# Kernel tuning notes

Hardware: AMD Instinct MI355X
Metric: run time of the kernel (lower is better)

Reference implementation:

```python
import jax, jax.numpy as jnp
import numpy as np

V, D, B, T = 50257, 512, 64, 512
MEM, FWD = 64, 48
RETRO = MEM - FWD  # 16
EPS = 1e-5


def setup_inputs() -> dict:
    key = jax.random.key(0)
    ks = jax.random.split(key, 16)
    n = lambda i, shape: (jax.random.normal(ks[i], shape, jnp.float32) * 0.02)
    return dict(
        seq=jax.random.randint(ks[0], (B, T), 0, V),
        embed=n(1, (V, D)),
        ff_w1=n(2, (D, 2 * D)), ff_b1=jnp.zeros((2 * D,), jnp.float32),
        ff_w2=n(3, (2 * D, D)), ff_b2=jnp.zeros((D,), jnp.float32),
        ln_g=jnp.ones((D,), jnp.float32), ln_b=jnp.zeros((D,), jnp.float32),
        fg_w=n(4, (D,)), fg_b=jnp.zeros((), jnp.float32),
        nw_w1=n(5, (2 * D, D)), nw_b1=jnp.zeros((D,), jnp.float32),
        nw_w2=n(6, (D,)), nw_b2=jnp.zeros((), jnp.float32),
        wq=n(7, (D, D)), bq=jnp.zeros((D,), jnp.float32),
        wk=n(8, (D, D)), bk=jnp.zeros((D,), jnp.float32),
        wv=n(9, (D, D)), bv=jnp.zeros((D,), jnp.float32),
        wo=n(10, (D, D)), bo=jnp.zeros((D,), jnp.float32),
        rq_w=n(11, (D, D)), rq_b=jnp.zeros((D,), jnp.float32),
        out_w=n(12, (D, V)), out_b=jnp.zeros((V,), jnp.float32),
    )


def reference(seq, embed, ff_w1, ff_b1, ff_w2, ff_b2, ln_g, ln_b,
              fg_w, fg_b, nw_w1, nw_b1, nw_w2, nw_b2,
              wq, bq, wk, bk, wv, bv, wo, bo, rq_w, rq_b, out_w, out_b):
    Bz = seq.shape[0]
    # Encoder: embed -> FFN residual -> LayerNorm
    h0 = embed[seq]                                            # [B,T,D]
    ff = jax.nn.relu(h0 @ ff_w1 + ff_b1) @ ff_w2 + ff_b2
    x = h0 + ff
    mu = x.mean(-1, keepdims=True)
    var = ((x - mu) ** 2).mean(-1, keepdims=True)
    hidden = (x - mu) / jnp.sqrt(var + EPS) * ln_g + ln_b       # [B,T,D]

    cand = hidden[:, :-3, :]                                   # [B,n_cand,D]
    n_cand = cand.shape[1]
    # Forward-gate topk (sorted ascending, as in torch code)
    fwd_scores = cand @ fg_w + fg_b                            # [B,n_cand]
    _, fwd_idx = jax.lax.top_k(fwd_scores, FWD)
    fwd_idx = jnp.sort(fwd_idx, axis=1)                        # [B,FWD]
    fwd_h = jnp.take_along_axis(hidden, fwd_idx[:, :, None], axis=1)  # [B,FWD,D]

    # Condition 'D': MHA re-encode (1 head) of forward slots over full sequence
    q = fwd_h @ wq + bq                                        # [B,FWD,D]
    kk = hidden @ wk + bk                                      # [B,T,D]
    v = hidden @ wv + bv                                       # [B,T,D]
    attn = jax.nn.softmax(jnp.einsum('bkd,btd->bkt', q, kk) / jnp.sqrt(jnp.float32(D)), axis=-1)
    re_slots = jnp.einsum('bkt,btd->bkd', attn, v) @ wo + bo   # [B,FWD,D]

    # New-write gate over skipped candidates -> retro slots
    context = hidden.mean(1)                                   # [B,D]
    gi = jnp.concatenate([cand, jnp.broadcast_to(context[:, None, :], cand.shape)], axis=-1)
    gs = jax.nn.sigmoid(jax.nn.relu(gi @ nw_w1 + nw_b1) @ nw_w2 + nw_b2)  # [B,n_cand]
    fwd_mask = jnp.zeros((Bz, n_cand), jnp.float32).at[
        jnp.arange(Bz)[:, None], fwd_idx].set(1.0)
    masked = jnp.where(fwd_mask > 0, -1e9, gs)
    _, sel = jax.lax.top_k(masked, RETRO)                      # [B,RETRO], descending-score order
    retro_h = jnp.take_along_axis(hidden, sel[:, :, None], axis=1)  # [B,RETRO,D]

    memory = jnp.concatenate([re_slots, retro_h], axis=1)      # [B,MEM,D] (exactly full)
    mem_mask = jnp.ones((Bz, MEM), jnp.float32)

    # Read head
    qh = hidden[:, -2, :] @ rq_w + rq_b                        # [B,D]
    scores = jnp.einsum('bmd,bd->bm', memory, qh)
    scores = jnp.where(mem_mask == 0, -1e9, scores)
    a = jax.nn.softmax(scores, axis=-1)
    ctx = jnp.einsum('bm,bmd->bd', a, memory)
    return ctx @ out_w + out_b                                 # [B,V]
```

## Files before the change

kernel.cpp:

```cpp
#include <hip/hip_runtime.h>

typedef unsigned short u16;
typedef unsigned int u32;

#define VV 50257
#define NCAND 509
#define NFWD 48
#define NRETRO 16

typedef __attribute__((ext_vector_type(8))) short bf16x8;
typedef __attribute__((ext_vector_type(4))) float f32x4;

__device__ __forceinline__ float bf2f(u16 u) {
  union { u32 i; float f; } v; v.i = ((u32)u) << 16; return v.f;
}
__device__ __forceinline__ u16 f2bf(float f) {
  union { float f; u32 u; } v; v.f = f;
  u32 u = v.u; u += 0x7fffu + ((u >> 16) & 1u); return (u16)(u >> 16);
}
__device__ __forceinline__ u16 bft(float f) {
  union { float f; u32 u; } v; v.f = f; return (u16)(v.u >> 16);
}
__device__ __forceinline__ float ldsel(const void* p, size_t i, int isbf) {
  return isbf ? bf2f(((const u16*)p)[i]) : ((const float*)p)[i];
}

__device__ __forceinline__ void g2l16(const u16* g, u16* l) {
  __builtin_amdgcn_global_load_lds((const __attribute__((address_space(1))) u32*)g,
                                   (__attribute__((address_space(3))) u32*)l, 16, 0, 0);
}

__global__ void detect_k(const u32* __restrict__ w, int* __restrict__ flag) {
  int bf = 1;
  for (int i = 0; i < 16; ++i) {
    u32 b1 = (w[i] >> 8) & 0x7fu;
    if (!(b1 >= 0x30u && b1 < 0x40u)) bf = 0;
  }
  *flag = bf;
}

__global__ void sentinel_k(float* __restrict__ out, int n, float val) {
  int i = blockIdx.x * 256 + threadIdx.x;
  if (i < n) out[i] = val;
}

__global__ __launch_bounds__(256) void tsplit_k(const float* __restrict__ W,
                                                u16* __restrict__ Th, u16* __restrict__ Tl,
                                                int K, int N) {
  __shared__ float tt[32][33];
  int nt = N >> 5;
  int n0 = (blockIdx.x % nt) << 5;
  int k0 = (blockIdx.x / nt) << 5;
  int c = threadIdx.x & 31, r = threadIdx.x >> 5;
#pragma unroll
  for (int i = 0; i < 32; i += 8) tt[r + i][c] = W[(size_t)(k0 + r + i) * N + n0 + c];
  __syncthreads();
#pragma unroll
  for (int i = 0; i < 32; i += 8) {
    int n = n0 + r + i, k = k0 + c;
    float v = tt[c][r + i];
    u16 h = bft(v);
    int idx = n * K + (k & ~63) + ((k & 63) ^ ((n & 7) << 3));
    Th[idx] = h; Tl[idx] = f2bf(v - bf2f(h));
  }
}

__global__ __launch_bounds__(256) void tout_k(const float* __restrict__ W,
                                              u16* __restrict__ WoT) {
  __shared__ float tt[32][33];
  const int nt = 1572;
  int n0 = (blockIdx.x % nt) << 5;
  int k0 = (blockIdx.x / nt) << 5;
  int c = threadIdx.x & 31, r = threadIdx.x >> 5;
#pragma unroll
  for (int i = 0; i < 32; i += 8) {
    int n = n0 + c;
    tt[r + i][c] = (n < VV) ? W[(size_t)(k0 + r + i) * VV + n] : 0.f;
  }
  __syncthreads();
#pragma unroll
  for (int i = 0; i < 32; i += 8) {
    int n = n0 + r + i, k = k0 + c;
    WoT[(size_t)n * 512 + (k & ~63) + ((k & 63) ^ ((n & 7) << 3))] = f2bf(tt[c][r + i]);
  }
}

__global__ void concat2_k(const float* __restrict__ a, const float* __restrict__ b,
                          float* __restrict__ o) {
  int i = blockIdx.x * 256 + threadIdx.x;
  if (i < 1024) o[i] = (i < 512) ? a[i] : b[i - 512];
}

__global__ __launch_bounds__(256) void gsplit_k(const float* __restrict__ embed,
                                                const int* __restrict__ seqp,
                                                u16* __restrict__ Ph, u16* __restrict__ Pl) {
  int g = blockIdx.x * 256 + threadIdx.x;
  int m = g >> 6, j8 = (g & 63) << 3;
  const float* s = embed + (size_t)seqp[m] * 512 + j8;
  float4 a = *(const float4*)s;
  float4 b = *(const float4*)(s + 4);
  u16 h0 = bft(a.x), h1 = bft(a.y), h2 = bft(a.z), h3 = bft(a.w);
  u16 h4 = bft(b.x), h5 = bft(b.y), h6 = bft(b.z), h7 = bft(b.w);
  uint4 hv, lv;
  hv.x = (u32)h0 | ((u32)h1 << 16); hv.y = (u32)h2 | ((u32)h3 << 16);
  hv.z = (u32)h4 | ((u32)h5 << 16); hv.w = (u32)h6 | ((u32)h7 << 16);
  lv.x = (u32)f2bf(a.x - bf2f(h0)) | ((u32)f2bf(a.y - bf2f(h1)) << 16);
  lv.y = (u32)f2bf(a.z - bf2f(h2)) | ((u32)f2bf(a.w - bf2f(h3)) << 16);
  lv.z = (u32)f2bf(b.x - bf2f(h4)) | ((u32)f2bf(b.y - bf2f(h5)) << 16);
  lv.w = (u32)f2bf(b.z - bf2f(h6)) | ((u32)f2bf(b.w - bf2f(h7)) << 16);
  int di = m * 512 + (j8 ^ ((m & 7) << 3));
  *(uint4*)&Ph[di] = hv;
  *(uint4*)&Pl[di] = lv;
}

template<int NT, int KST, int ADDM, int RELU, int OUT>
__global__ __launch_bounds__(256) void mgemm_k(
    const u16* __restrict__ Ah, const u16* __restrict__ Al,
    const u16* __restrict__ Bh, const u16* __restrict__ Bl,
    int lda, int ldb, int koff,
    const float* __restrict__ biasf, int boff,
    const u16* __restrict__ Rh, const u16* __restrict__ Rl,
    const float* __restrict__ addf,
    float* __restrict__ Cf, u16* __restrict__ Cb,
    u16* __restrict__ Ohi, u16* __restrict__ Olo, int ldc)
{
  __shared__ __align__(16) u16 lds[32768];
  int tid = threadIdx.x;
  int cpx = gridDim.x >> 3;
  int bid = blockIdx.x;
  int wg = (bid & 7) * cpx + (bid >> 3);
  int my = wg / NT, nx = wg % NT;
  int m0 = my << 7, n0 = nx << 7;
  int lane = tid & 63, wid = tid >> 6;

  const u16* gw; int stw;
  if (wid == 0)      { gw = Ah + (size_t)m0 * lda;        stw = lda; }
  else if (wid == 1) { gw = Al + (size_t)m0 * lda;        stw = lda; }
  else if (wid == 2) { gw = Bh + (size_t)n0 * ldb + koff; stw = ldb; }
  else               { gw = Bl + (size_t)n0 * ldb + koff; stw = ldb; }
  const u16* gl = gw + (size_t)(lane >> 3) * stw + ((lane & 7) << 3);
  int lb = wid << 13;

  f32x4 acc[4][4] = {};
  int wr = wid >> 1, wc = wid & 1;
  int cl = lane & 15;
  int kq8 = (lane >> 4) << 3;
  int swz = (cl & 7) << 3;

  for (int k0 = 0; k0 < KST * 64; k0 += 64) {
#pragma unroll
    for (int i = 0; i < 16; ++i)
      g2l16(gl + (size_t)(i << 3) * stw + k0, &lds[lb + (i << 9)]);
    __syncthreads();
#pragma unroll
    for (int kt = 0; kt < 2; ++kt) {
      int kA = ((kt << 5) + kq8) ^ swz;
      bf16x8 bh[4], blo[4];
#pragma unroll
      for (int i = 0; i < 4; ++i) {
        int ib = (((wc << 6) + (i << 4) + cl) << 6) + kA;
        bh[i]  = *(const bf16x8*)&lds[16384 + ib];
        blo[i] = *(const bf16x8*)&lds[24576 + ib];
      }
#pragma unroll
      for (int i2 = 0; i2 < 4; ++i2) {
        int ia = (((wr << 6) + (i2 << 4) + cl) << 6) + kA;
        bf16x8 ah  = *(const bf16x8*)&lds[ia];
        bf16x8 alo = *(const bf16x8*)&lds[8192 + ia];
#pragma unroll
        for (int j = 0; j < 4; ++j) {
          acc[i2][j] = __builtin_amdgcn_mfma_f32_16x16x32_bf16(ah,  bh[j],  acc[i2][j], 0, 0, 0);
          acc[i2][j] = __builtin_amdgcn_mfma_f32_16x16x32_bf16(alo, bh[j],  acc[i2][j], 0, 0, 0);
          acc[i2][j] = __builtin_amdgcn_mfma_f32_16x16x32_bf16(ah,  blo[j], acc[i2][j], 0, 0, 0);
        }
      }
    }
    __syncthreads();
  }

  int rq = (lane >> 4) << 2;
  int mb = m0 + (wr << 6);
  int nb = n0 + (wc << 6);
#pragma unroll
  for (int j = 0; j < 4; ++j) {
    int n = nb + (j << 4) + cl;
    float bi = biasf ? biasf[boff + n] : 0.f;
#pragma unroll
    for (int i2 = 0; i2 < 4; ++i2) {
#pragma unroll
      for (int r = 0; r < 4; ++r) {
        int m = mb + (i2 << 4) + rq + r;
        float v = acc[i2][j][r] + bi;
        if (ADDM == 1) {
          int ridx = m * 512 + (n ^ ((m & 7) << 3));
          v += bf2f(Rh[ridx]) + bf2f(Rl[ridx]);
        }
        if (ADDM == 2) v += addf[((m >> 9) << 9) + n];
        if (RELU) v = fmaxf(v, 0.f);
        if (OUT == 0) Cf[(size_t)m * ldc + n] = v;
        else if (OUT == 1) Cb[(size_t)m * ldc + n] = f2bf(v);
        else if (OUT == 2) {
          u16 h = bft(v);
          size_t oidx = (size_t)m * ldc + (n & ~63) + ((n & 63) ^ ((m & 7) << 3));
          Ohi[oidx] = h; Olo[oidx] = f2bf(v - bf2f(h));
        } else {
          int r64 = (m * 43691) >> 21;
          int mm = (r64 << 6) + (m - r64 * 48);
          Cf[(size_t)mm * 512 + n] = v;
        }
      }
    }
  }
}

__global__ __launch_bounds__(256) void out_mgemm_k(
    const u16* __restrict__ ctxh, const u16* __restrict__ ctxl,
    const u16* __restrict__ WoT, const float* __restrict__ ob,
    float* __restrict__ out) {
  __shared__ __align__(16) u16 lds[16384];
  int tid = threadIdx.x;
  int n0 = blockIdx.x << 7;
  int lane = tid & 63, wid = tid >> 6;
  const u16* gw; int lb0;
  if (wid == 0)      { gw = ctxh;                         lb0 = 0; }
  else if (wid == 1) { gw = ctxl;                         lb0 = 4096; }
  else if (wid == 2) { gw = WoT + (size_t)n0 * 512;        lb0 = 8192; }
  else               { gw = WoT + (size_t)(n0 + 64) * 512; lb0 = 12288; }
  const u16* gl = gw + (size_t)(lane >> 3) * 512 + ((lane & 7) << 3);

  f32x4 acc[4][2] = {};
  int cl = lane & 15;
  int kq8 = (lane >> 4) << 3;
  int swz = (cl & 7) << 3;

  for (int k0 = 0; k0 < 512; k0 += 64) {
#pragma unroll
    for (int i = 0; i < 8; ++i)
      g2l16(gl + (size_t)(i << 3) * 512 + k0, &lds[lb0 + (i << 9)]);
    __syncthreads();
#pragma unroll
    for (int kt = 0; kt < 2; ++kt) {
      int kA = ((kt << 5) + kq8) ^ swz;
      bf16x8 bw[2];
#pragma unroll
      for (int j = 0; j < 2; ++j) {
        int rB = (wid << 5) + (j << 4) + cl;
        bw[j] = *(const bf16x8*)&lds[8192 + (rB << 6) + kA];
      }
#pragma unroll
      for (int i2 = 0; i2 < 4; ++i2) {
        int ra = ((i2 << 4) + cl) << 6;
        bf16x8 ah  = *(const bf16x8*)&lds[ra + kA];
        bf16x8 alo = *(const bf16x8*)&lds[4096 + ra + kA];
#pragma unroll
        for (int j = 0; j < 2; ++j) {
          acc[i2][j] = __builtin_amdgcn_mfma_f32_16x16x32_bf16(ah,  bw[j], acc[i2][j], 0, 0, 0);
          acc[i2][j] = __builtin_amdgcn_mfma_f32_16x16x32_bf16(alo, bw[j], acc[i2][j], 0, 0, 0);
        }
      }
    }
    __syncthreads();
  }

  int rq = (lane >> 4) << 2;
#pragma unroll
  for (int j = 0; j < 2; ++j) {
    int n = n0 + (wid << 5) + (j << 4) + cl;
    if (n < VV) {
      float bi = ob[n];
#pragma unroll
      for (int i2 = 0; i2 < 4; ++i2)
#pragma unroll
        for (int r = 0; r < 4; ++r)
          out[(size_t)((i2 << 4) + rq + r) * VV + n] = acc[i2][j][r] + bi;
    }
  }
}

template<int AG, int ADDM, int RELU, int ACC, int OUTBF>
__global__ __launch_bounds__(256) void gemm_k(
    const float* __restrict__ A, int lda,
    const void* __restrict__ gbase, const int* __restrict__ gidx,
    const void* __restrict__ Bw, int ldb, size_t boff,
    const void* __restrict__ bias, size_t bias_eoff,
    const void* __restrict__ adg_base, const int* __restrict__ adg_idx, int adg_ld,
    const float* __restrict__ addf, int add_shift, int addf_ld,
    void* __restrict__ Cv, int ldc, int K,
    const int* __restrict__ flagp)
{
  __shared__ float As[16][68];
  __shared__ float Bs[16][68];
  int isbf = *flagp;
  int tid = threadIdx.x;
  int m0 = blockIdx.y * 64;
  int n0 = blockIdx.x * 64;
  int tx = tid & 15, ty = tid >> 4;
  int arow = tid >> 2;
  int akq  = (tid & 3) << 2;
  int bcol = tid & 63;
  int bk0  = tid >> 6;

  size_t a_off = (size_t)(m0 + arow) * (size_t)lda;
  float acc[4][4] = {};

  for (int k0 = 0; k0 < K; k0 += 16) {
    {
      float4 v = *(const float4*)(A + a_off + k0 + akq);
      As[akq + 0][arow] = v.x;
      As[akq + 1][arow] = v.y;
      As[akq + 2][arow] = v.z;
      As[akq + 3][arow] = v.w;
    }
    if (isbf) {
      const u16* bp = (const u16*)Bw + boff;
#pragma unroll
      for (int l = 0; l < 4; ++l) {
        int kb = bk0 + (l << 2);
        Bs[kb][bcol] = bf2f(bp[(size_t)(k0 + kb) * ldb + n0 + bcol]);
      }
    } else {
      const float* bp = (const float*)Bw + boff;
#pragma unroll
      for (int l = 0; l < 4; ++l) {
        int kb = bk0 + (l << 2);
        Bs[kb][bcol] = bp[(size_t)(k0 + kb) * ldb + n0 + bcol];
      }
    }
    __syncthreads();
#pragma unroll
    for (int k = 0; k < 16; ++k) {
      float4 a4 = *(const float4*)&As[k][ty << 2];
      float4 b4 = *(const float4*)&Bs[k][tx << 2];
      float a[4] = {a4.x, a4.y, a4.z, a4.w};
      float bv[4] = {b4.x, b4.y, b4.z, b4.w};
#pragma unroll
      for (int i = 0; i < 4; ++i)
#pragma unroll
        for (int j = 0; j < 4; ++j) acc[i][j] += a[i] * bv[j];
    }
    __syncthreads();
  }

  int mrow = m0 + (ty << 2);
  int ncol = n0 + (tx << 2);
  float bi4[4] = {0.f, 0.f, 0.f, 0.f};
  if (bias) {
#pragma unroll
    for (int j = 0; j < 4; ++j) bi4[j] = ldsel(bias, bias_eoff + ncol + j, isbf);
  }
#pragma unroll
  for (int i = 0; i < 4; ++i) {
    int m = mrow + i;
    float v[4];
#pragma unroll
    for (int j = 0; j < 4; ++j) v[j] = acc[i][j] + bi4[j];
    if (RELU) {
#pragma unroll
      for (int j = 0; j < 4; ++j) v[j] = fmaxf(v[j], 0.f);
    }
    float4 o; o.x = v[0]; o.y = v[1]; o.z = v[2]; o.w = v[3];
    *(float4*)((float*)Cv + (size_t)m * ldc + ncol) = o;
  }
}

__global__ __launch_bounds__(256) void ln_split_k(const float* __restrict__ x,
                                                  const float* __restrict__ g,
                                                  const float* __restrict__ bt,
                                                  u16* __restrict__ Hh, u16* __restrict__ Hl) {
  int row = blockIdx.x;
  const float* p = x + (size_t)row * 512;
  int tid = threadIdx.x;
  __shared__ float red[256];
  __shared__ float stat[2];
  float v0 = p[tid], v1 = p[tid + 256];
  red[tid] = v0 + v1;
  __syncthreads();
  for (int s = 128; s > 0; s >>= 1) { if (tid < s) red[tid] += red[tid + s]; __syncthreads(); }
  if (tid == 0) stat[0] = red[0] * (1.0f / 512.0f);
  __syncthreads();
  float mu = stat[0];
  float d0 = v0 - mu, d1 = v1 - mu;
  red[tid] = d0 * d0 + d1 * d1;
  __syncthreads();
  for (int s = 128; s > 0; s >>= 1) { if (tid < s) red[tid] += red[tid + s]; __syncthreads(); }
  if (tid == 0) stat[1] = 1.0f / sqrtf(red[0] * (1.0f / 512.0f) + 1e-5f);
  __syncthreads();
  float inv = stat[1];
  float y0 = d0 * inv * g[tid] + bt[tid];
  float y1 = d1 * inv * g[tid + 256] + bt[tid + 256];
  int c = (row & 7) << 3;
  int i0 = row * 512 + (tid ^ c);
  int i1 = row * 512 + ((tid + 256) ^ c);
  u16 h0 = bft(y0), h1 = bft(y1);
  Hh[i0] = h0; Hl[i0] = f2bf(y0 - bf2f(h0));
  Hh[i1] = h1; Hl[i1] = f2bf(y1 - bf2f(h1));
}

__global__ __launch_bounds__(256) void gatectx_k(const u16* __restrict__ Hh,
                                                 const u16* __restrict__ Hl,
                                                 const float* __restrict__ w,
                                                 const float* __restrict__ b,
                                                 float* __restrict__ out,
                                                 float* __restrict__ part) {
  int bb = blockIdx.y, t0 = blockIdx.x * 64;
  __shared__ float wl[512];
  __shared__ float cred[4][512];
  for (int d = threadIdx.x; d < 512; d += 256) wl[d] = w[d];
  int wave = threadIdx.x >> 6, lane = threadIdx.x & 63;
  float ca[8] = {};
  __syncthreads();
  float bias = b[0];
  for (int r = wave; r < 64; r += 4) {
    int grow = bb * 512 + t0 + r;
    int lx = lane ^ ((grow & 7) << 3);
    const u16* ph = Hh + (size_t)grow * 512;
    const u16* pl = Hl + (size_t)grow * 512;
    float s = 0.f;
#pragma unroll
    for (int d = 0; d < 8; ++d) {
      float hv = bf2f(ph[lx + d * 64]) + bf2f(pl[lx + d * 64]);
      ca[d] += hv;
      s += hv * wl[lane + d * 64];
    }
#pragma unroll
    for (int off = 32; off > 0; off >>= 1) s += __shfl_xor(s, off);
    if (lane == 0) out[bb * 512 + t0 + r] = s + bias;
  }
#pragma unroll
  for (int d = 0; d < 8; ++d) cred[wave][lane + d * 64] = ca[d];
  __syncthreads();
  for (int d = threadIdx.x; d < 512; d += 256)
    part[(size_t)((bb << 3) + blockIdx.x) * 512 + d] =
        cred[0][d] + cred[1][d] + cred[2][d] + cred[3][d];
}

template<int SIG>
__global__ __launch_bounds__(256) void score_k(const float* __restrict__ h,
                                               const void* __restrict__ w,
                                               const void* __restrict__ b,
                                               float* __restrict__ out,
                                               const int* __restrict__ flagp) {
  int isbf = *flagp;
  int bb = blockIdx.y; int t0 = blockIdx.x * 64;
  __shared__ float wl[512];
  for (int d = threadIdx.x; d < 512; d += 256) wl[d] = ldsel(w, d, isbf);
  __syncthreads();
  int wave = threadIdx.x >> 6, lane = threadIdx.x & 63;
  float bias = ldsel(b, 0, isbf);
  for (int r = wave; r < 64; r += 4) {
    const float* hp = h + ((size_t)bb * 512 + t0 + r) * 512;
    float s = 0.f;
#pragma unroll
    for (int d = 0; d < 8; ++d) s += hp[lane + d * 64] * wl[lane + d * 64];
#pragma unroll
    for (int off = 32; off > 0; off >>= 1) s += __shfl_xor(s, off);
    if (lane == 0) {
      float v = s + bias;
      if (SIG) v = 1.0f / (1.0f + expf(-v));
      out[bb * 512 + t0 + r] = v;
    }
  }
}

__global__ __launch_bounds__(256) void topk_fwd_k(const float* __restrict__ scores,
                                                  int* __restrict__ fwd_idx,
                                                  int* __restrict__ fwd_mask) {
  int b = blockIdx.x, tid = threadIdx.x;
  __shared__ float sv[512];
  __shared__ int flg[512];
  for (int t = tid; t < 512; t += 256)
    sv[t] = (t < NCAND) ? scores[b * 512 + t] : -3.0e38f;
  __syncthreads();
  const float4* sv4 = (const float4*)sv;
#pragma unroll
  for (int h = 0; h < 2; ++h) {
    int t = tid + (h << 8);
    float s = sv[t];
    int cnt = 0;
    for (int t2 = 0; t2 < 128; ++t2) {
      float4 o = sv4[t2];
      int base = t2 << 2;
      cnt += (o.x > s) || (o.x == s && (base + 0) < t);
      cnt += (o.y > s) || (o.y == s && (base + 1) < t);
      cnt += (o.z > s) || (o.z == s && (base + 2) < t);
      cnt += (o.w > s) || (o.w == s && (base + 3) < t);
    }
    int f = (cnt < NFWD) ? 1 : 0;
    flg[t] = f;
    fwd_mask[b * 512 + t] = f;
  }
  __syncthreads();
#pragma unroll
  for (int h = 0; h < 2; ++h) {
    int t = tid + (h << 8);
    if (flg[t]) {
      int pos = 0;
      for (int t2 = 0; t2 < t; ++t2) pos += flg[t2];
      fwd_idx[b * NFWD + pos] = t;
    }
  }
}

__global__ __launch_bounds__(256) void topk_retro_k(const float* __restrict__ gs,
                                                    const int* __restrict__ fwd_mask,
                                                    int* __restrict__ sel) {
  int b = blockIdx.x, tid = threadIdx.x;
  __shared__ float sv[512];
  for (int t = tid; t < 512; t += 256) {
    float v;
    if (t < NCAND) v = fwd_mask[b * 512 + t] ? -1.0e9f : gs[b * 512 + t];
    else v = -3.0e38f;
    sv[t] = v;
  }
  __syncthreads();
  const float4* sv4 = (const float4*)sv;
#pragma unroll
  for (int h = 0; h < 2; ++h) {
    int t = tid + (h << 8);
    float s = sv[t];
    int cnt = 0;
    for (int t2 = 0; t2 < 128; ++t2) {
      float4 o = sv4[t2];
      int base = t2 << 2;
      cnt += (o.x > s) || (o.x == s && (base + 0) < t);
      cnt += (o.y > s) || (o.y == s && (base + 1) < t);
      cnt += (o.z > s) || (o.z == s && (base + 2) < t);
      cnt += (o.w > s) || (o.w == s && (base + 3) < t);
    }
    if (cnt < NRETRO) sel[b * NRETRO + cnt] = t;
  }
}

__global__ __launch_bounds__(512) void context_red_k(const float* __restrict__ part,
                                                     float* __restrict__ ctx) {
  int b = blockIdx.x, d = threadIdx.x;
  float s = 0.f;
#pragma unroll
  for (int c = 0; c < 8; ++c) s += part[(size_t)((b << 3) + c) * 512 + d];
  ctx[b * 512 + d] = s * (1.0f / 512.0f);
}

__global__ __launch_bounds__(256) void fwdh_gather_p(const u16* __restrict__ Hh,
                                                     const u16* __restrict__ Hl,
                                                     const int* __restrict__ fwd_idx,
                                                     u16* __restrict__ Fh, u16* __restrict__ Fl) {
  int idx = blockIdx.x * 256 + threadIdx.x;
  int d = idx & 511, r = idx >> 9;
  int b = r / NFWD, i = r % NFWD;
  int t = fwd_idx[b * NFWD + i];
  int srow = b * 512 + t;
  int si = srow * 512 + (d & ~63) + ((d & 63) ^ ((srow & 7) << 3));
  float v = bf2f(Hh[si]) + bf2f(Hl[si]);
  u16 h = bft(v);
  int di = r * 512 + (d & ~63) + ((d & 63) ^ ((r & 7) << 3));
  Fh[di] = h; Fl[di] = f2bf(v - bf2f(h));
}

__global__ __launch_bounds__(256) void retro_gather_p(const u16* __restrict__ Hh,
                                                      const u16* __restrict__ Hl,
                                                      const int* __restrict__ sel,
                                                      float* __restrict__ mem) {
  int idx = blockIdx.x * 256 + threadIdx.x;
  int d = idx & 511, r = idx >> 9, b = r >> 4, j = r & 15;
  int t = sel[b * NRETRO + j];
  int srow = b * 512 + t;
  int si = srow * 512 + (d & ~63) + ((d & 63) ^ ((srow & 7) << 3));
  mem[((size_t)b * 64 + NFWD + j) * 512 + d] = bf2f(Hh[si]) + bf2f(Hl[si]);
}

__global__ __launch_bounds__(256) void s_k(const float* __restrict__ q,
                                           const u16* __restrict__ kk,
                                           float* __restrict__ S) {
  int b = blockIdx.y, t0 = blockIdx.x * 64;
  int tid = threadIdx.x, tq = tid & 15, kq = tid >> 4;
  __shared__ float qs[16][49];
  __shared__ float ks[16][68];
  float acc[3][4] = {};
  for (int dc = 0; dc < 512; dc += 16) {
    for (int e = tid; e < 768; e += 256) {
      int d = e / 48, k2 = e % 48;
      qs[d][k2] = q[((size_t)b * 48 + k2) * 512 + dc + d];
    }
    for (int e = tid; e < 1024; e += 256) {
      int t = e >> 4, d = e & 15;
      ks[d][t] = bf2f(kk[((size_t)b * 512 + t0 + t) * 1024 + dc + d]);
    }
    __syncthreads();
#pragma unroll
    for (int d = 0; d < 16; ++d) {
      float4 kv = *(const float4*)&ks[d][tq << 2];
#pragma unroll
      for (int j = 0; j < 3; ++j) {
        float qv = qs[d][kq * 3 + j];
        acc[j][0] += qv * kv.x; acc[j][1] += qv * kv.y;
        acc[j][2] += qv * kv.z; acc[j][3] += qv * kv.w;
      }
    }
    __syncthreads();
  }
  const float sc = 0.044194173824159216f;
#pragma unroll
  for (int j = 0; j < 3; ++j) {
    int k = kq * 3 + j;
    float4 o; o.x = acc[j][0] * sc; o.y = acc[j][1] * sc;
    o.z = acc[j][2] * sc; o.w = acc[j][3] * sc;
    *(float4*)&S[((size_t)b * 48 + k) * 512 + t0 + (tq << 2)] = o;
  }
}

__global__ __launch_bounds__(256) void softmax_k(float* __restrict__ S) {
  float* p = S + (size_t)blockIdx.x * 512;
  int tid = threadIdx.x;
  __shared__ float red[256];
  __shared__ float stat[2];
  float v0 = p[tid], v1 = p[tid + 256];
  red[tid] = fmaxf(v0, v1);
  __syncthreads();
  for (int s = 128; s > 0; s >>= 1) { if (tid < s) red[tid] = fmaxf(red[tid], red[tid + s]); __syncthreads(); }
  if (tid == 0) stat[0] = red[0];
  __syncthreads();
  float mx = stat[0];
  float e0 = expf(v0 - mx), e1 = expf(v1 - mx);
  red[tid] = e0 + e1;
  __syncthreads();
  for (int s = 128; s > 0; s >>= 1) { if (tid < s) red[tid] += red[tid + s]; __syncthreads(); }
  if (tid == 0) stat[1] = 1.0f / red[0];
  __syncthreads();
  float inv = stat[1];
  p[tid] = e0 * inv; p[tid + 256] = e1 * inv;
}

__global__ __launch_bounds__(256) void pv_k(const float* __restrict__ P,
                                            const u16* __restrict__ vvp,
                                            u16* __restrict__ Ph, u16* __restrict__ Pl) {
  int b = blockIdx.y, d0 = blockIdx.x * 64;
  int tid = threadIdx.x, dq = tid & 15, kq = tid >> 4;
  __shared__ float ps[16][49];
  __shared__ float vs[16][68];
  float acc[3][4] = {};
  for (int tc = 0; tc < 512; tc += 16) {
    for (int e = tid; e < 768; e += 256) {
      int t = e / 48, k2 = e % 48;
      ps[t][k2] = P[((size_t)b * 48 + k2) * 512 + tc + t];
    }
    for (int e = tid; e < 1024; e += 256) {
      int t = e >> 6, d = e & 63;
      vs[t][d] = bf2f(vvp[((size_t)b * 512 + tc + t) * 1024 + d0 + d]);
    }
    __syncthreads();
#pragma unroll
    for (int t = 0; t < 16; ++t) {
      float4 vval = *(const float4*)&vs[t][dq << 2];
#pragma unroll
      for (int j = 0; j < 3; ++j) {
        float pp = ps[t][kq * 3 + j];
        acc[j][0] += pp * vval.x; acc[j][1] += pp * vval.y;
        acc[j][2] += pp * vval.z; acc[j][3] += pp * vval.w;
      }
    }
    __syncthreads();
  }
#pragma unroll
  for (int j = 0; j < 3; ++j) {
    int k = kq * 3 + j;
    int row = b * 48 + k;
    int c = (row & 7) << 3;
    int di = row * 512 + d0 + ((dq << 2) ^ c);
    float v0 = acc[j][0], v1 = acc[j][1], v2 = acc[j][2], v3 = acc[j][3];
    u16 h0 = bft(v0), h1 = bft(v1), h2 = bft(v2), h3 = bft(v3);
    uint2 hv, lv;
    hv.x = (u32)h0 | ((u32)h1 << 16); hv.y = (u32)h2 | ((u32)h3 << 16);
    lv.x = (u32)f2bf(v0 - bf2f(h0)) | ((u32)f2bf(v1 - bf2f(h1)) << 16);
    lv.y = (u32)f2bf(v2 - bf2f(h2)) | ((u32)f2bf(v3 - bf2f(h3)) << 16);
    *(uint2*)&Ph[di] = hv;
    *(uint2*)&Pl[di] = lv;
  }
}

__global__ __launch_bounds__(512) void qh_p_k(const u16* __restrict__ Hh,
                                              const u16* __restrict__ Hl,
                                              const float* __restrict__ rq_w,
                                              const float* __restrict__ rq_b,
                                              float* __restrict__ qh) {
  int b = blockIdx.x, d = threadIdx.x;
  __shared__ float hr[512];
  int row = b * 512 + 510;
  int idx = row * 512 + (d & ~63) + ((d & 63) ^ 48);
  hr[d] = bf2f(Hh[idx]) + bf2f(Hl[idx]);
  __syncthreads();
  float s = 0.f;
  for (int k = 0; k < 512; ++k) s += hr[k] * rq_w[(size_t)k * 512 + d];
  qh[b * 512 + d] = s + rq_b[d];
}

__global__ __launch_bounds__(512) void mem_attn_k(const float* __restrict__ mem,
                                                  const float* __restrict__ qh,
                                                  u16* __restrict__ ctxh,
                                                  u16* __restrict__ ctxl) {
  int b = blockIdx.x, tid = threadIdx.x;
  __shared__ float qv[512];
  __shared__ float sc[64];
  qv[tid] = qh[b * 512 + tid];
  __syncthreads();
  if (tid < 64) {
    const float* mp = mem + ((size_t)b * 64 + tid) * 512;
    float s = 0.f;
    for (int d = 0; d < 512; ++d) s += mp[d] * qv[d];
    float mx = s;
#pragma unroll
    for (int off = 32; off > 0; off >>= 1) mx = fmaxf(mx, __shfl_xor(mx, off));
    float e = expf(s - mx);
    float sum = e;
#pragma unroll
    for (int off = 32; off > 0; off >>= 1) sum += __shfl_xor(sum, off);
    sc[tid] = e / sum;
  }
  __syncthreads();
  float a = 0.f;
  for (int m = 0; m < 64; ++m) a += sc[m] * mem[((size_t)b * 64 + m) * 512 + tid];
  int di = b * 512 + (tid & ~63) + ((tid & 63) ^ ((b & 7) << 3));
  u16 h = bft(a);
  ctxh[di] = h; ctxl[di] = f2bf(a - bf2f(h));
}

extern "C" void kernel_launch(void* const* d_in, const int* in_sizes, int n_in,
                              void* d_out, int out_size, void* d_ws, size_t ws_size,
                              hipStream_t stream) {
  const int*  seq    = (const int*)d_in[0];
  const void* embed  = d_in[1];
  const void* ff_w1  = d_in[2];
  const void* ff_b1  = d_in[3];
  const void* ff_w2  = d_in[4];
  const void* ff_b2  = d_in[5];
  const void* ln_g   = d_in[6];
  const void* ln_b   = d_in[7];
  const void* fg_w   = d_in[8];
  const void* fg_b   = d_in[9];
  const void* nw_w1  = d_in[10];
  const void* nw_b1  = d_in[11];
  const void* nw_w2  = d_in[12];
  const void* nw_b2  = d_in[13];
  const void* wq     = d_in[14];
  const void* bq     = d_in[15];
  const void* wk     = d_in[16];
  const void* bk     = d_in[17];
  const void* wv     = d_in[18];
  const void* bv     = d_in[19];
  const void* wo     = d_in[20];
  const void* bo     = d_in[21];
  const void* rq_w   = d_in[22];
  const void* rq_b   = d_in[23];
  const void* out_w  = d_in[24];
  const void* out_b  = d_in[25];
  float* out = (float*)d_out;

  float* ws = (float*)d_ws;
  float* hidden = ws;
  float* g1f    = ws;
  u16*   kvu    = (u16*)ws;
  u16* h0h   = (u16*)(ws + 16777216);
  u16* h0l   = h0h + 4194304;
  u16* actHh = (u16*)(ws + 20971520);
  u16* actHl = actHh + 8388608;
  u16* Hh    = (u16*)(ws + 16777216);
  u16* Hl    = Hh + 16777216;
  u16* WoT   = (u16*)(ws + 16777216);
  size_t S0 = 33554432;
  float* fwd_scores = ws + S0;
  float* gs         = ws + S0 + 32768;
  float* context    = ws + S0 + 65536;
  float* gate_bias  = ws + S0 + 98304;
  float* qh         = ws + S0 + 131072;
  u16*   ctxh       = (u16*)(ws + S0 + 163840);
  u16*   ctxl       = ctxh + 32768;
  int*   fwd_idx    = (int*)(ws + S0 + 196608);
  int*   sel        = (int*)(ws + S0 + 199680);
  int*   fwd_mask   = (int*)(ws + S0 + 200704);
  int*   flagp      = (int*)(ws + S0 + 233472);
  float* bkv        = ws + S0 + 236544;
  float* cpart      = ws + S0 + 262144;
  u16*   Fh         = (u16*)(ws + S0 + 262144);
  u16*   Fl         = Fh + 1572864;
  float* q          = ws + S0 + 1835008;
  float* Smat       = ws + S0 + 3407872;
  u16* W0    = (u16*)(ws + S0 + 3407872);
  u16* WTnh  = W0;            u16* WTnl  = W0 + 262144;
  u16* WTkvh = W0 + 524288;   u16* WTkvl = W0 + 1048576;
  u16* WT1h  = W0 + 1572864;  u16* WT1l  = W0 + 2097152;
  u16* WT2h  = W0 + 2621440;  u16* WT2l  = W0 + 3145728;
  u16* Ph    = (u16*)(ws + S0 + 4980736);
  u16* Pl    = Ph + 1572864;
  u16* Wq0   = (u16*)(ws + S0 + 6553600);
  u16* WTqh  = Wq0;          u16* WTql = Wq0 + 262144;
  u16* WToh  = Wq0 + 524288; u16* WTol = Wq0 + 786432;
  float* memory = ws + S0 + 8126464;
  const size_t NEED = (size_t)(33554432 + 10223616) * 4;

  if (ws_size < NEED) {
    float val = 500.0f + (float)(ws_size >> 20);
    sentinel_k<<<(out_size + 255) / 256, 256, 0, stream>>>(out, out_size, val);
    return;
  }

  detect_k<<<1, 1, 0, stream>>>((const u32*)embed, flagp);

  tsplit_k<<<512, 256, 0, stream>>>((const float*)ff_w1, WT1h, WT1l, 512, 1024);
  tsplit_k<<<512, 256, 0, stream>>>((const float*)ff_w2, WT2h, WT2l, 1024, 512);
  tsplit_k<<<256, 256, 0, stream>>>((const float*)nw_w1, WTnh, WTnl, 512, 512);
  tsplit_k<<<256, 256, 0, stream>>>((const float*)wk, WTkvh, WTkvl, 512, 512);
  tsplit_k<<<256, 256, 0, stream>>>((const float*)wv, WTkvh + 512*512, WTkvl + 512*512, 512, 512);
  tsplit_k<<<256, 256, 0, stream>>>((const float*)wq, WTqh, WTql, 512, 512);
  tsplit_k<<<256, 256, 0, stream>>>((const float*)wo, WToh, WTol, 512, 512);
  concat2_k<<<4, 256, 0, stream>>>((const float*)bk, (const float*)bv, bkv);

  for (int mc = 0; mc < 4; ++mc) {
    const int* seqp = seq + mc * 8192;
    float* hid = hidden + (size_t)mc * 8192 * 512;
    gsplit_k<<<2048, 256, 0, stream>>>((const float*)embed, seqp, h0h, h0l);
    mgemm_k<8,8,0,1,2><<<512, 256, 0, stream>>>(
        h0h, h0l, WT1h, WT1l, 512, 512, 0,
        (const float*)ff_b1, 0, nullptr, nullptr, nullptr,
        nullptr, nullptr, actHh, actHl, 1024);
    mgemm_k<4,16,1,0,0><<<256, 256, 0, stream>>>(
        actHh, actHl, WT2h, WT2l, 1024, 1024, 0,
        (const float*)ff_b2, 0, h0h, h0l, nullptr,
        hid, nullptr, nullptr, nullptr, 512);
  }
  ln_split_k<<<32768, 256, 0, stream>>>(hidden, (const float*)ln_g, (const float*)ln_b, Hh, Hl);
  gatectx_k<<<dim3(8,64), 256, 0, stream>>>(Hh, Hl, (const float*)fg_w, (const float*)fg_b,
                                            fwd_scores, cpart);
  topk_fwd_k<<<64, 256, 0, stream>>>(fwd_scores, fwd_idx, fwd_mask);
  context_red_k<<<64, 512, 0, stream>>>(cpart, context);
  gemm_k<0,0,0,0,0><<<dim3(8,1), 256, 0, stream>>>(
      context, 512, nullptr, nullptr, nw_w1, 512, (size_t)512*512, nw_b1, 0,
      nullptr, nullptr, 0, nullptr, 0, 0, gate_bias, 512, 512, flagp);
  mgemm_k<4,8,2,1,0><<<1024, 256, 0, stream>>>(
      Hh, Hl, WTnh, WTnl, 512, 512, 0,
      nullptr, 0, nullptr, nullptr, gate_bias,
      g1f, nullptr, nullptr, nullptr, 512);
  score_k<1><<<dim3(8,64), 256, 0, stream>>>(g1f, nw_w2, nw_b2, gs, flagp);
  topk_retro_k<<<64, 256, 0, stream>>>(gs, fwd_mask, sel);
  retro_gather_p<<<2048, 256, 0, stream>>>(Hh, Hl, sel, memory);
  fwdh_gather_p<<<6144, 256, 0, stream>>>(Hh, Hl, fwd_idx, Fh, Fl);
  mgemm_k<4,8,0,0,0><<<96, 256, 0, stream>>>(
      Fh, Fl, WTqh, WTql, 512, 512, 0,
      (const float*)bq, 0, nullptr, nullptr, nullptr,
      q, nullptr, nullptr, nullptr, 512);
  mgemm_k<8,8,0,0,1><<<2048, 256, 0, stream>>>(
      Hh, Hl, WTkvh, WTkvl, 512, 512, 0,
      bkv, 0, nullptr, nullptr, nullptr,
      nullptr, kvu, nullptr, nullptr, 1024);
  s_k<<<dim3(8,64), 256, 0, stream>>>(q, kvu, Smat);
  softmax_k<<<3072, 256, 0, stream>>>(Smat);
  pv_k<<<dim3(8,64), 256, 0, stream>>>(Smat, kvu + 512, Ph, Pl);
  mgemm_k<4,8,0,0,3><<<96, 256, 0, stream>>>(
      Ph, Pl, WToh, WTol, 512, 512, 0,
      (const float*)bo, 0, nullptr, nullptr, nullptr,
      memory, nullptr, nullptr, nullptr, 512);
  qh_p_k<<<64, 512, 0, stream>>>(Hh, Hl, (const float*)rq_w, (const float*)rq_b, qh);
  mem_attn_k<<<64, 512, 0, stream>>>(memory, qh, ctxh, ctxl);
  tout_k<<<16 * 1572, 256, 0, stream>>>((const float*)out_w, WoT);
  out_mgemm_k<<<393, 256, 0, stream>>>(ctxh, ctxl, WoT, (const float*)out_b, out);
}
```

Before: 1.193 ms.

## Halve mgemm N-tile to 64 and fuse gate score dot into GEMM epilogue

The shared split-bf16 MFMA GEMM now uses 128x64 tiles instead of 128x128. That doubles the grid of every GEMM launch and cuts LDS use, so more blocks can be resident. A new epilogue mode for the new-write gate multiplies the relu'd hidden activations by nw_w2 and reduces them across lanes and waves into per-tile partial sums. A small reduction kernel then applies the bias and sigmoid, which removes the 2048x... g1f store and the separate score_k pass. The smaller tile lowers MFMA work per LDS load and re-reads the A operand twice as often, which may hurt the large FFN and KV GEMMs.

```diff
diff --git a/kernel.cpp b/kernel.cpp
--- a/kernel.cpp
+++ b/kernel.cpp
@@ -121,46 +121,52 @@
     const float* __restrict__ biasf, int boff,
     const u16* __restrict__ Rh, const u16* __restrict__ Rl,
     const float* __restrict__ addf,
+    const float* __restrict__ w2g, float* __restrict__ gpart,
     float* __restrict__ Cf, u16* __restrict__ Cb,
     u16* __restrict__ Ohi, u16* __restrict__ Olo, int ldc)
 {
-  __shared__ __align__(16) u16 lds[32768];
+  __shared__ __align__(16) u16 lds[24576];
   int tid = threadIdx.x;
   int cpx = gridDim.x >> 3;
   int bid = blockIdx.x;
   int wg = (bid & 7) * cpx + (bid >> 3);
   int my = wg / NT, nx = wg % NT;
-  int m0 = my << 7, n0 = nx << 7;
+  int m0 = my << 7, n0 = nx << 6;
   int lane = tid & 63, wid = tid >> 6;
 
-  const u16* gw; int stw;
-  if (wid == 0)      { gw = Ah + (size_t)m0 * lda;        stw = lda; }
-  else if (wid == 1) { gw = Al + (size_t)m0 * lda;        stw = lda; }
-  else if (wid == 2) { gw = Bh + (size_t)n0 * ldb + koff; stw = ldb; }
-  else               { gw = Bl + (size_t)n0 * ldb + koff; stw = ldb; }
+  const u16* gw; int stw; int lb;
+  if (wid == 0)      { gw = Ah + (size_t)m0 * lda;        stw = lda; lb = 0; }
+  else if (wid == 1) { gw = Al + (size_t)m0 * lda;        stw = lda; lb = 8192; }
+  else if (wid == 2) { gw = Bh + (size_t)n0 * ldb + koff; stw = ldb; lb = 16384; }
+  else               { gw = Bl + (size_t)n0 * ldb + koff; stw = ldb; lb = 20480; }
   const u16* gl = gw + (size_t)(lane >> 3) * stw + ((lane & 7) << 3);
-  int lb = wid << 13;
-
-  f32x4 acc[4][4] = {};
+
+  f32x4 acc[4][2] = {};
   int wr = wid >> 1, wc = wid & 1;
   int cl = lane & 15;
   int kq8 = (lane >> 4) << 3;
   int swz = (cl & 7) << 3;
 
   for (int k0 = 0; k0 < KST * 64; k0 += 64) {
-#pragma unroll
-    for (int i = 0; i < 16; ++i)
-      g2l16(gl + (size_t)(i << 3) * stw + k0, &lds[lb + (i << 9)]);
+    if (wid < 2) {
+#pragma unroll
+      for (int i = 0; i < 16; ++i)
+        g2l16(gl + (size_t)(i << 3) * stw + k0, &lds[lb + (i << 9)]);
+    } else {
+#pragma unroll
+      for (int i = 0; i < 8; ++i)
+        g2l16(gl + (size_t)(i << 3) * stw + k0, &lds[lb + (i << 9)]);
+    }
     __syncthreads();
 #pragma unroll
     for (int kt = 0; kt < 2; ++kt) {
       int kA = ((kt << 5) + kq8) ^ swz;
-      bf16x8 bh[4], blo[4];
-#pragma unroll
-      for (int i = 0; i < 4; ++i) {
-        int ib = (((wc << 6) + (i << 4) + cl) << 6) + kA;
-        bh[i]  = *(const bf16x8*)&lds[16384 + ib];
-        blo[i] = *(const bf16x8*)&lds[24576 + ib];
+      bf16x8 bh[2], blo[2];
+#pragma unroll
+      for (int j = 0; j < 2; ++j) {
+        int ib = (((wc << 5) + (j << 4) + cl) << 6) + kA;
+        bh[j]  = *(const bf16x8*)&lds[16384 + ib];
+        blo[j] = *(const bf16x8*)&lds[20480 + ib];
       }
 #pragma unroll
       for (int i2 = 0; i2 < 4; ++i2) {
@@ -168,7 +174,7 @@
         bf16x8 ah  = *(const bf16x8*)&lds[ia];
         bf16x8 alo = *(const bf16x8*)&lds[8192 + ia];
 #pragma unroll
-        for (int j = 0; j < 4; ++j) {
+        for (int j = 0; j < 2; ++j) {
           acc[i2][j] = __builtin_amdgcn_mfma_f32_16x16x32_bf16(ah,  bh[j],  acc[i2][j], 0, 0, 0);
           acc[i2][j] = __builtin_amdgcn_mfma_f32_16x16x32_bf16(alo, bh[j],  acc[i2][j], 0, 0, 0);
           acc[i2][j] = __builtin_amdgcn_mfma_f32_16x16x32_bf16(ah,  blo[j], acc[i2][j], 0, 0, 0);
@@ -180,9 +186,59 @@
 
   int rq = (lane >> 4) << 2;
   int mb = m0 + (wr << 6);
-  int nb = n0 + (wc << 6);
-#pragma unroll
-  for (int j = 0; j < 4; ++j) {
+  int nb = n0 + (wc << 5);
+
+  if (OUT == 4) {
+    float rs[4][4];
+#pragma unroll
+    for (int i2 = 0; i2 < 4; ++i2)
+#pragma unroll
+      for (int r = 0; r < 4; ++r) rs[i2][r] = 0.f;
+#pragma unroll
+    for (int j = 0; j < 2; ++j) {
+      int n = nb + (j << 4) + cl;
+      float w2 = w2g[n];
+      float bi = biasf ? biasf[boff + n] : 0.f;
+#pragma unroll
+      for (int i2 = 0; i2 < 4; ++i2) {
+#pragma unroll
+        for (int r = 0; r < 4; ++r) {
+          int m = mb + (i2 << 4) + rq + r;
+          float v = acc[i2][j][r] + bi;
+          if (ADDM == 2) v += addf[((m >> 9) << 9) + n];
+          if (RELU) v = fmaxf(v, 0.f);
+          rs[i2][r] += v * w2;
+        }
+      }
+    }
+#pragma unroll
+    for (int i2 = 0; i2 < 4; ++i2)
+#pragma unroll
+      for (int r = 0; r < 4; ++r) {
+        float s = rs[i2][r];
+#pragma unroll
+        for (int off = 8; off > 0; off >>= 1) s += __shfl_xor(s, off);
+        rs[i2][r] = s;
+      }
+    float* lf = (float*)lds;
+    if (cl == 0) {
+#pragma unroll
+      for (int i2 = 0; i2 < 4; ++i2)
+#pragma unroll
+        for (int r = 0; r < 4; ++r)
+          lf[(wr << 7) + (wc << 6) + (i2 << 4) + rq + r] = rs[i2][r];
+    }
+    __syncthreads();
+    if (tid < 128) {
+      int w = tid >> 6, m64 = tid & 63;
+      float s = lf[(w << 7) + m64] + lf[(w << 7) + 64 + m64];
+      gpart[(size_t)(m0 + (w << 6) + m64) * NT + nx] = s;
+    }
+    return;
+  }
+
+#pragma unroll
+  for (int j = 0; j < 2; ++j) {
     int n = nb + (j << 4) + cl;
     float bi = biasf ? biasf[boff + n] : 0.f;
 #pragma unroll
@@ -211,6 +267,18 @@
       }
     }
   }
+}
+
+__global__ __launch_bounds__(256) void gs_red_k(const float* __restrict__ gpart,
+                                                const float* __restrict__ b2,
+                                                float* __restrict__ gs) {
+  int m = blockIdx.x * 256 + threadIdx.x;
+  const float* p = gpart + (size_t)m * 8;
+  float t = 0.f;
+#pragma unroll
+  for (int i = 0; i < 8; ++i) t += p[i];
+  float s = t + b2[0];
+  gs[m] = 1.0f / (1.0f + expf(-s));
 }
 
 __global__ __launch_bounds__(256) void out_mgemm_k(
@@ -432,34 +500,6 @@
   for (int d = threadIdx.x; d < 512; d += 256)
     part[(size_t)((bb << 3) + blockIdx.x) * 512 + d] =
         cred[0][d] + cred[1][d] + cred[2][d] + cred[3][d];
-}
-
-template<int SIG>
-__global__ __launch_bounds__(256) void score_k(const float* __restrict__ h,
-                                               const void* __restrict__ w,
-                                               const void* __restrict__ b,
-                                               float* __restrict__ out,
-                                               const int* __restrict__ flagp) {
-  int isbf = *flagp;
-  int bb = blockIdx.y; int t0 = blockIdx.x * 64;
-  __shared__ float wl[512];
-  for (int d = threadIdx.x; d < 512; d += 256) wl[d] = ldsel(w, d, isbf);
-  __syncthreads();
-  int wave = threadIdx.x >> 6, lane = threadIdx.x & 63;
-  float bias = ldsel(b, 0, isbf);
-  for (int r = wave; r < 64; r += 4) {
-    const float* hp = h + ((size_t)bb * 512 + t0 + r) * 512;
-    float s = 0.f;
-#pragma unroll
-    for (int d = 0; d < 8; ++d) s += hp[lane + d * 64] * wl[lane + d * 64];
-#pragma unroll
-    for (int off = 32; off > 0; off >>= 1) s += __shfl_xor(s, off);
-    if (lane == 0) {
-      float v = s + bias;
-      if (SIG) v = 1.0f / (1.0f + expf(-v));
-      out[bb * 512 + t0 + r] = v;
-    }
-  }
 }
 
 __global__ __launch_bounds__(256) void topk_fwd_k(const float* __restrict__ scores,
@@ -756,7 +796,6 @@
 
   float* ws = (float*)d_ws;
   float* hidden = ws;
-  float* g1f    = ws;
   u16*   kvu    = (u16*)ws;
   u16* h0h   = (u16*)(ws + 16777216);
   u16* h0l   = h0h + 4194304;
@@ -779,6 +818,7 @@
   int*   flagp      = (int*)(ws + S0 + 233472);
   float* bkv        = ws + S0 + 236544;
   float* cpart      = ws + S0 + 262144;
+  float* gpart      = ws + S0 + 262144;
   u16*   Fh         = (u16*)(ws + S0 + 262144);
   u16*   Fl         = Fh + 1572864;
   float* q          = ws + S0 + 1835008;
@@ -817,13 +857,15 @@
     const int* seqp = seq + mc * 8192;
     float* hid = hidden + (size_t)mc * 8192 * 512;
     gsplit_k<<<2048, 256, 0, stream>>>((const float*)embed, seqp, h0h, h0l);
-    mgemm_k<8,8,0,1,2><<<512, 256, 0, stream>>>(
+    mgemm_k<16,8,0,1,2><<<1024, 256, 0, stream>>>(
         h0h, h0l, WT1h, WT1l, 512, 512, 0,
         (const float*)ff_b1, 0, nullptr, nullptr, nullptr,
+        nullptr, nullptr,
         nullptr, nullptr, actHh, actHl, 1024);
-    mgemm_k<4,16,1,0,0><<<256, 256, 0, stream>>>(
+    mgemm_k<8,16,1,0,0><<<512, 256, 0, stream>>>(
         actHh, actHl, WT2h, WT2l, 1024, 1024, 0,
         (const float*)ff_b2, 0, h0h, h0l, nullptr,
+        nullptr, nullptr,
         hid, nullptr, nullptr, nullptr, 512);
   }
   ln_split_k<<<32768, 256, 0, stream>>>(hidden, (const float*)ln_g, (const float*)ln_b, Hh, Hl);
@@ -834,28 +876,32 @@
   gemm_k<0,0,0,0,0><<<dim3(8,1), 256, 0, stream>>>(
       context, 512, nullptr, nullptr, nw_w1, 512, (size_t)512*512, nw_b1, 0,
       nullptr, nullptr, 0, nullptr, 0, 0, gate_bias, 512, 512, flagp);
-  mgemm_k<4,8,2,1,0><<<1024, 256, 0, stream>>>(
+  mgemm_k<8,8,2,1,4><<<2048, 256, 0, stream>>>(
       Hh, Hl, WTnh, WTnl, 512, 512, 0,
       nullptr, 0, nullptr, nullptr, gate_bias,
-      g1f, nullptr, nullptr, nullptr, 512);
-  score_k<1><<<dim3(8,64), 256, 0, stream>>>(g1f, nw_w2, nw_b2, gs, flagp);
+      (const float*)nw_w2, gpart,
+      nullptr, nullptr, nullptr, nullptr, 512);
+  gs_red_k<<<128, 256, 0, stream>>>(gpart, (const float*)nw_b2, gs);
   topk_retro_k<<<64, 256, 0, stream>>>(gs, fwd_mask, sel);
   retro_gather_p<<<2048, 256, 0, stream>>>(Hh, Hl, sel, memory);
   fwdh_gather_p<<<6144, 256, 0, stream>>>(Hh, Hl, fwd_idx, Fh, Fl);
-  mgemm_k<4,8,0,0,0><<<96, 256, 0, stream>>>(
+  mgemm_k<8,8,0,0,0><<<192, 256, 0, stream>>>(
       Fh, Fl, WTqh, WTql, 512, 512, 0,
       (const float*)bq, 0, nullptr, nullptr, nullptr,
+      nullptr, nullptr,
       q, nullptr, nullptr, nullptr, 512);
-  mgemm_k<8,8,0,0,1><<<2048, 256, 0, stream>>>(
+  mgemm_k<16,8,0,0,1><<<4096, 256, 0, stream>>>(
       Hh, Hl, WTkvh, WTkvl, 512, 512, 0,
       bkv, 0, nullptr, nullptr, nullptr,
+      nullptr, nullptr,
       nullptr, kvu, nullptr, nullptr, 1024);
   s_k<<<dim3(8,64), 256, 0, stream>>>(q, kvu, Smat);
   softmax_k<<<3072, 256, 0, stream>>>(Smat);
   pv_k<<<dim3(8,64), 256, 0, stream>>>(Smat, kvu + 512, Ph, Pl);
-  mgemm_k<4,8,0,0,3><<<96, 256, 0, stream>>>(
+  mgemm_k<8,8,0,0,3><<<192, 256, 0, stream>>>(
       Ph, Pl, WToh, WTol, 512, 512, 0,
       (const float*)bo, 0, nullptr, nullptr, nullptr,
+      nullptr, nullptr,
       memory, nullptr, nullptr, nullptr, 512);
   qh_p_k<<<64, 512, 0, stream>>>(Hh, Hl, (const float*)rq_w, (const float*)rq_b, qh);
   mem_attn_k<<<64, 512, 0, stream>>>(memory, qh, ctxh, ctxl);
```

New measurement: 1.160 ms. -2.7%, faster.
